# Performance work log

Measured on AMD Instinct MI355X. Metric: run time of the kernel, lower is better.

Reference implementation:

```python
import jax, jax.numpy as jnp
import numpy as np

E_DIM = 64
N_EMBED = 8192

def setup_inputs() -> dict:
    key = jax.random.key(0)
    k1, k2 = jax.random.split(key)
    x = jax.random.normal(k1, (16, E_DIM, 32, 32), dtype=jnp.float32)   # [B, e_dim, H, W]
    embed = jax.random.normal(k2, (E_DIM, N_EMBED), dtype=jnp.float32)  # codebook [e_dim, n_embed]
    return {"x": x, "embed": embed}

def reference(x, embed):
    e_dim, n_embed = embed.shape
    # NCHW -> NHWC
    xp = jnp.transpose(x, (0, 2, 3, 1))              # [B, H, W, e_dim]
    flat = xp.reshape(-1, e_dim)                     # [N, e_dim]
    # squared-distance expansion: ||f||^2 - 2 f.E + ||e||^2  -> [N, n_embed]
    distance = (jnp.sum(flat * flat, axis=1, keepdims=True)
                - 2.0 * flat @ embed
                + jnp.sum(embed * embed, axis=0, keepdims=True))
    embed_idx = jnp.argmax(-distance, axis=1)        # [N] nearest code ids
    embed_idx = embed_idx.reshape(xp.shape[:-1])     # [B, H, W]
    # gather codes: embedding table is embed.T -> [n_embed, e_dim]
    quantize = jnp.take(embed.T, embed_idx, axis=0)  # [B, H, W, e_dim]
    return quantize
```

## Files before the change

kernel.cpp:

```cpp
#include <hip/hip_runtime.h>


typedef __attribute__((ext_vector_type(8))) __bf16 bf16x8;
typedef __attribute__((ext_vector_type(4))) float f32x4;
typedef unsigned int u32;
typedef unsigned long long u64;

union frag_cast { f32x4 f; bf16x8 b; };
__device__ __forceinline__ bf16x8 as_bf16x8(f32x4 v) { frag_cast u; u.f = v; return u.b; }

#define N_ROWS  16384
#define E_DIM   64
#define N_EMBED 8192
#define NCHUNK  16
#define COLS_PER_BLOCK (N_EMBED / NCHUNK)
#define N_ST (COLS_PER_BLOCK / 64)
#define ROWS_PER_BLOCK 256
#define N_ROWBLK (N_ROWS / ROWS_PER_BLOCK)
#define MARGIN_THR 2e-3f

#define WS_AH   0u
#define WS_AL   (2u << 20)
#define WS_B    (4u << 20)
#define WS_ET   (6u << 20)
#define WS_BIAS (8u << 20)
#define WS_PB1  (WS_BIAS + (64u << 10))
#define WS_PI1  (WS_PB1 + (1u << 20))
#define WS_PB2  (WS_PI1 + (1u << 20))
#define WS_FIDX (WS_PB2 + (1u << 20))
#define WS_FLAG (WS_FIDX + (64u << 10))
#define WS_CNT  (WS_FLAG + (64u << 10))
#define WS_FKEY (WS_CNT + (4u << 10))

__device__ __forceinline__ u32 f32_key(float s) {
    u32 u = __float_as_uint(s);
    return (u & 0x80000000u) ? ~u : (u | 0x80000000u);
}

__device__ __forceinline__ void async16(const void* g, void* l) {
    __builtin_amdgcn_global_load_lds(
        (const __attribute__((address_space(1))) void*)g,
        (__attribute__((address_space(3))) void*)l, 16, 0, 0);
}

__global__ __launch_bounds__(256) void prep(
        const float* __restrict__ x, const float* __restrict__ embed, char* ws) {
    __shared__ float tile[64][65];
    __bf16* Ah = (__bf16*)(ws + WS_AH);
    __bf16* Al = (__bf16*)(ws + WS_AL);
    float*  eT = (float*)(ws + WS_ET);
    float*  bias = (float*)(ws + WS_BIAS);
    const int t = threadIdx.x;
    const int blk = blockIdx.x;

    if (blk < 256) {
        const int b = blk >> 4, p0 = (blk & 15) * 64;
        {
            const int c = t >> 2, seg = (t & 3) * 16;
            const float* src = x + b * 65536 + c * 1024 + p0 + seg;
#pragma unroll
            for (int i = 0; i < 16; ++i) tile[c][seg + i] = src[i];
        }
        __syncthreads();
        const int p = t >> 2, cq = (t & 3) * 16;
        const long row = b * 1024 + p0 + p;
        bf16x8 vh0, vh1, vl0, vl1;
#pragma unroll
        for (int i = 0; i < 16; ++i) {
            float f = tile[cq + i][p];
            __bf16 h = (__bf16)f;
            __bf16 l = (__bf16)(f - (float)h);
            if (i < 8) { vh0[i] = h; vl0[i] = l; }
            else       { vh1[i - 8] = h; vl1[i - 8] = l; }
        }
        *(bf16x8*)(Ah + row * 64 + cq) = vh0;
        *(bf16x8*)(Ah + row * 64 + cq + 8) = vh1;
        *(bf16x8*)(Al + row * 64 + cq) = vl0;
        *(bf16x8*)(Al + row * 64 + cq + 8) = vl1;
    } else {
        if (blk == 256 && t == 0) *(int*)(ws + WS_CNT) = 0;
        const int g = blk - 256;
        const int jbase = g * 64;
        char* Bg = ws + WS_B + (size_t)g * 16384;
        {
            const int c = t >> 2, seg = (t & 3) * 16;
            const float* src = embed + c * N_EMBED + jbase + seg;
#pragma unroll
            for (int i = 0; i < 16; ++i) tile[c][seg + i] = src[i];
        }
        __syncthreads();
        if (t < 64) {
            float s = 0.f;
#pragma unroll
            for (int c = 0; c < 64; ++c) { float v = tile[c][t]; s = fmaf(v, v, s); }
            bias[jbase + t] = -0.5f * s;
        }
        const int jl = t >> 2, cq = (t & 3) * 16;
        bf16x8 vh0, vh1, vl0, vl1;
#pragma unroll
        for (int i = 0; i < 16; ++i) {
            float f = tile[cq + i][jl];
            eT[(long)(jbase + jl) * 64 + cq + i] = f;
            __bf16 h = (__bf16)f;
            __bf16 l = (__bf16)(f - (float)h);
            if (i < 8) { vh0[i] = h; vl0[i] = l; }
            else       { vh1[i - 8] = h; vl1[i - 8] = l; }
        }
        const int k0 = (cq >> 3), sw = jl & 7;
        __bf16* hi = (__bf16*)Bg + jl * 64;
        __bf16* lo = (__bf16*)(Bg + 8192) + jl * 64;
        *(bf16x8*)(hi + ((k0 ^ sw) * 8))       = vh0;
        *(bf16x8*)(hi + (((k0 + 1) ^ sw) * 8)) = vh1;
        *(bf16x8*)(lo + ((k0 ^ sw) * 8))       = vl0;
        *(bf16x8*)(lo + (((k0 + 1) ^ sw) * 8)) = vl1;
    }
}

__global__ __launch_bounds__(256, 4) void qdist(const char* __restrict__ ws_c, char* __restrict__ ws) {
    __shared__ __align__(16) char smem[2][16384];
    const __bf16* Ah = (const __bf16*)(ws_c + WS_AH);
    const __bf16* Al = (const __bf16*)(ws_c + WS_AL);
    const char* Bws = ws_c + WS_B;
    const float* biasg = (const float*)(ws_c + WS_BIAS);
    float* pb1 = (float*)(ws + WS_PB1);
    int*   pi1 = (int*)(ws + WS_PI1);
    float* pb2 = (float*)(ws + WS_PB2);

    const int t = threadIdx.x;
    const int wv = t >> 6, lane = t & 63, ln = lane & 15, q = lane >> 4;
    const int rb = blockIdx.x >> 4, chunk = blockIdx.x & 15;
    const int row0 = rb * ROWS_PER_BLOCK;
    const int col0 = chunk * COLS_PER_BLOCK;
    const int g0 = col0 >> 6;

    f32x4 pfh[4][2], pfl[4][2];
#pragma unroll
    for (int nt = 0; nt < 4; ++nt) {
        long row = row0 + wv * 64 + nt * 16 + ln;
        long base = row * 64 + q * 8;
        pfh[nt][0] = *(const f32x4*)(Ah + base);
        pfh[nt][1] = *(const f32x4*)(Ah + base + 32);
        pfl[nt][0] = *(const f32x4*)(Al + base);
        pfl[nt][1] = *(const f32x4*)(Al + base + 32);
    }
    asm volatile("" :
        "+v"(pfh[0][0]), "+v"(pfh[0][1]), "+v"(pfh[1][0]), "+v"(pfh[1][1]),
        "+v"(pfh[2][0]), "+v"(pfh[2][1]), "+v"(pfh[3][0]), "+v"(pfh[3][1]),
        "+v"(pfl[0][0]), "+v"(pfl[0][1]), "+v"(pfl[1][0]), "+v"(pfl[1][1]),
        "+v"(pfl[2][0]), "+v"(pfl[2][1]), "+v"(pfl[3][0]), "+v"(pfl[3][1]));

    float b1[4], b2[4]; int iq[4];
#pragma unroll
    for (int k = 0; k < 4; ++k) { b1[k] = -3.4e38f; b2[k] = -3.4e38f; iq[k] = 0; }

    const int s7 = ln & 7;
    const int rdbase = ln * 128 + ((q ^ s7) << 4);

    auto issue = [&](int st) {
        const char* src = Bws + (size_t)(g0 + st) * 16384;
        char* dst = smem[st & 1];
#pragma unroll
        for (int s = 0; s < 4; ++s)
            async16(src + s * 4096 + wv * 1024 + lane * 16,
                    dst + s * 4096 + wv * 1024);
    };

    issue(0);
    for (int st = 0; st < N_ST; ++st) {
        __syncthreads();
        if (st + 1 < N_ST) issue(st + 1);
        const char* buf = smem[st & 1];
#pragma unroll
        for (int ct = 0; ct < 4; ++ct) {
            const int boff = ct * 2048 + rdbase;
            bf16x8 ah0 = *(const bf16x8*)(buf + boff);
            bf16x8 ah1 = *(const bf16x8*)(buf + (boff ^ 64));
            bf16x8 al0 = *(const bf16x8*)(buf + 8192 + boff);
            bf16x8 al1 = *(const bf16x8*)(buf + 8192 + (boff ^ 64));
            const int cbase = col0 + st * 64 + ct * 16;
            f32x4 bv = *(const f32x4*)(biasg + cbase + q * 4);
            const int jq = cbase + q * 4;
#pragma unroll
            for (int nt = 0; nt < 4; ++nt) {
                f32x4 acc = __builtin_amdgcn_mfma_f32_16x16x32_bf16(al0, as_bf16x8(pfh[nt][0]), bv, 0, 0, 0);
                acc = __builtin_amdgcn_mfma_f32_16x16x32_bf16(al1, as_bf16x8(pfh[nt][1]), acc, 0, 0, 0);
                acc = __builtin_amdgcn_mfma_f32_16x16x32_bf16(ah0, as_bf16x8(pfl[nt][0]), acc, 0, 0, 0);
                acc = __builtin_amdgcn_mfma_f32_16x16x32_bf16(ah1, as_bf16x8(pfl[nt][1]), acc, 0, 0, 0);
                acc = __builtin_amdgcn_mfma_f32_16x16x32_bf16(ah0, as_bf16x8(pfh[nt][0]), acc, 0, 0, 0);
                acc = __builtin_amdgcn_mfma_f32_16x16x32_bf16(ah1, as_bf16x8(pfh[nt][1]), acc, 0, 0, 0);
                float mx = fmaxf(fmaxf(acc[0], acc[1]), fmaxf(acc[2], acc[3]));
                b2[nt] = fmaxf(b2[nt], fminf(b1[nt], mx));
                bool gt = mx > b1[nt];
                b1[nt] = fmaxf(b1[nt], mx);
                iq[nt] = gt ? jq : iq[nt];
            }
        }
    }

#pragma unroll
    for (int m = 16; m < 64; m <<= 1) {
#pragma unroll
        for (int nt = 0; nt < 4; ++nt) {
            float o1 = __shfl_xor(b1[nt], m);
            int   oi = __shfl_xor(iq[nt], m);
            float o2 = __shfl_xor(b2[nt], m);
            b2[nt] = fmaxf(fmaxf(fminf(b1[nt], o1), o2), b2[nt]);
            bool take = (o1 > b1[nt]) || (o1 == b1[nt] && oi < iq[nt]);
            if (take) { b1[nt] = o1; iq[nt] = oi; }
        }
    }
    if (q == 0) {
#pragma unroll
        for (int nt = 0; nt < 4; ++nt) {
            int pixel = row0 + wv * 64 + nt * 16 + ln;
            int o = chunk * N_ROWS + pixel;
            pb1[o] = b1[nt];
            pi1[o] = iq[nt];
            pb2[o] = b2[nt];
        }
    }
}

__global__ __launch_bounds__(256) void reduce_rows(const float* __restrict__ x, char* ws) {
    const float* pb1 = (const float*)(ws + WS_PB1);
    const int*   pi1 = (const int*)(ws + WS_PI1);
    const float* pb2 = (const float*)(ws + WS_PB2);
    const float* eT = (const float*)(ws + WS_ET);
    const float* bias = (const float*)(ws + WS_BIAS);
    int* fidx = (int*)(ws + WS_FIDX);
    int* flags = (int*)(ws + WS_FLAG);
    int* cnt = (int*)(ws + WS_CNT);
    u64* fkey = (u64*)(ws + WS_FKEY);
    const int row = blockIdx.x * 256 + threadIdx.x;

    float b1 = pb1[row]; int iq = pi1[row]; float b2 = pb2[row];
#pragma unroll
    for (int ch = 1; ch < NCHUNK; ++ch) {
        float o1 = pb1[ch * N_ROWS + row];
        int   oi = pi1[ch * N_ROWS + row];
        float o2 = pb2[ch * N_ROWS + row];
        b2 = fmaxf(fmaxf(fminf(b1, o1), o2), b2);
        if (o1 > b1 || (o1 == b1 && oi < iq)) { b1 = o1; iq = oi; }
    }

    if (b1 - b2 < MARGIN_THR) {
        fidx[row] = -1;
        fkey[row] = 0ull;
        flags[atomicAdd(cnt, 1)] = row;
    } else {
        float xr[64];
        const float* xb = x + (row >> 10) * 65536 + (row & 1023);
#pragma unroll
        for (int c = 0; c < 64; ++c) xr[c] = xb[c * 1024];
        float best = -3.4e38f; int bi = iq;
#pragma unroll
        for (int cc = 0; cc < 4; ++cc) {
            const int j = iq + cc;
            const float* e = eT + j * 64;
            float s = bias[j];
#pragma unroll
            for (int c = 0; c < 64; ++c) s = fmaf(xr[c], e[c], s);
            if (s > best) { best = s; bi = j; }
        }
        fidx[row] = bi;
    }
}

__global__ __launch_bounds__(256) void recheck(const float* __restrict__ x, char* ws) {
    __shared__ float fl[64];
    __shared__ u64 red[256];
    const float* eT = (const float*)(ws + WS_ET);
    const float* bias = (const float*)(ws + WS_BIAS);
    const int* flags = (const int*)(ws + WS_FLAG);
    const int n = *(const int*)(ws + WS_CNT);
    u64* fkey = (u64*)(ws + WS_FKEY);
    const int t = threadIdx.x;
    const int seg = blockIdx.x & 31;
    const int rstep = gridDim.x >> 5;
    const int j = seg * 256 + t;

    for (int rowi = blockIdx.x >> 5; rowi < n; rowi += rstep) {
        const int row = flags[rowi];
        __syncthreads();
        if (t < 64) fl[t] = x[(row >> 10) * 65536 + t * 1024 + (row & 1023)];
        __syncthreads();
        float xr[64];
#pragma unroll
        for (int c = 0; c < 64; ++c) xr[c] = fl[c];

        const f32x4* e = (const f32x4*)(eT + (size_t)j * 64);
        f32x4 a0 = {0.f, 0.f, 0.f, 0.f}, a1 = a0, a2 = a0, a3 = a0;
#pragma unroll
        for (int v = 0; v < 4; ++v) {
            f32x4 e0 = e[v * 4 + 0], e1 = e[v * 4 + 1];
            f32x4 e2 = e[v * 4 + 2], e3 = e[v * 4 + 3];
#pragma unroll
            for (int k = 0; k < 4; ++k) {
                a0[k] = fmaf(xr[v * 16 + k],      e0[k], a0[k]);
                a1[k] = fmaf(xr[v * 16 + 4 + k],  e1[k], a1[k]);
                a2[k] = fmaf(xr[v * 16 + 8 + k],  e2[k], a2[k]);
                a3[k] = fmaf(xr[v * 16 + 12 + k], e3[k], a3[k]);
            }
        }
        f32x4 a01 = a0 + a1, a23 = a2 + a3;
        f32x4 as = a01 + a23;
        float s = bias[j] + ((as[0] + as[1]) + (as[2] + as[3]));

        red[t] = ((u64)f32_key(s) << 32) | (u32)(~(u32)j);
        __syncthreads();
        for (int off = 128; off; off >>= 1) {
            if (t < off) { u64 o = red[t + off]; if (o > red[t]) red[t] = o; }
            __syncthreads();
        }
        if (t == 0) atomicMax(&fkey[row], red[0]);
        __syncthreads();
    }
}

__global__ __launch_bounds__(256) void gather_out(const char* __restrict__ ws,
                                                  float* __restrict__ out) {
    const int* fidx = (const int*)(ws + WS_FIDX);
    const u64* fkey = (const u64*)(ws + WS_FKEY);
    const float* eT = (const float*)(ws + WS_ET);
    int g = blockIdx.x * 256 + threadIdx.x;
    int row = g >> 6, c = g & 63;
    int idx = fidx[row];
    if (idx < 0) idx = (int)(~(u32)(fkey[row] & 0xffffffffull));
    out[g] = eT[idx * 64 + c];
}

extern "C" void kernel_launch(void* const* d_in, const int* in_sizes, int n_in,
                              void* d_out, int out_size, void* d_ws, size_t ws_size,
                              hipStream_t stream) {
    const float* x     = (const float*)d_in[0];
    const float* embed = (const float*)d_in[1];
    float* out = (float*)d_out;
    char* ws = (char*)d_ws;

    prep<<<384, 256, 0, stream>>>(x, embed, ws);
    qdist<<<N_ROWBLK * NCHUNK, 256, 0, stream>>>(ws, ws);
    reduce_rows<<<N_ROWS / 256, 256, 0, stream>>>(x, ws);
    recheck<<<2048, 256, 0, stream>>>(x, ws);
    gather_out<<<(N_ROWS * 64) / 256, 256, 0, stream>>>(ws, out);
}
```

Baseline: 137.7 us.

## Fuse row reduction into qdist via last-block-done ticket counter

Removes the separate reduce_rows kernel. Each qdist block now takes a ticket from a per-row-block atomic counter after writing its partial argmax results, and the last of the 16 chunk blocks for a row block performs the cross-chunk reduction, margin check and fp32 refinement. This drops one kernel launch and its launch gap, and lets the reduction overlap with other qdist blocks still running. In exchange it adds a threadfence, an atomic and extra register pressure to qdist, and the reduction work is serialized onto whichever block finishes last.

```diff
diff --git a/kernel.cpp b/kernel.cpp
--- a/kernel.cpp
+++ b/kernel.cpp
@@ -31,6 +31,7 @@
 #define WS_FLAG (WS_FIDX + (64u << 10))
 #define WS_CNT  (WS_FLAG + (64u << 10))
 #define WS_FKEY (WS_CNT + (4u << 10))
+#define WS_DONE (WS_FKEY + (128u << 10))
 
 __device__ __forceinline__ u32 f32_key(float s) {
     u32 u = __float_as_uint(s);
@@ -78,7 +79,10 @@
         *(bf16x8*)(Al + row * 64 + cq) = vl0;
         *(bf16x8*)(Al + row * 64 + cq + 8) = vl1;
     } else {
-        if (blk == 256 && t == 0) *(int*)(ws + WS_CNT) = 0;
+        if (blk == 256) {
+            if (t == 0) *(int*)(ws + WS_CNT) = 0;
+            if (t < N_ROWBLK) ((int*)(ws + WS_DONE))[t] = 0;
+        }
         const int g = blk - 256;
         const int jbase = g * 64;
         char* Bg = ws + WS_B + (size_t)g * 16384;
@@ -116,8 +120,11 @@
     }
 }
 
-__global__ __launch_bounds__(256, 4) void qdist(const char* __restrict__ ws_c, char* __restrict__ ws) {
+__global__ __launch_bounds__(256, 4) void qdist(const float* __restrict__ x,
+                                                const char* __restrict__ ws_c,
+                                                char* __restrict__ ws) {
     __shared__ __align__(16) char smem[2][16384];
+    __shared__ int ticket_s;
     const __bf16* Ah = (const __bf16*)(ws_c + WS_AH);
     const __bf16* Al = (const __bf16*)(ws_c + WS_AL);
     const char* Bws = ws_c + WS_B;
@@ -219,50 +226,51 @@
             pb2[o] = b2[nt];
         }
     }
-}
-
-__global__ __launch_bounds__(256) void reduce_rows(const float* __restrict__ x, char* ws) {
-    const float* pb1 = (const float*)(ws + WS_PB1);
-    const int*   pi1 = (const int*)(ws + WS_PI1);
-    const float* pb2 = (const float*)(ws + WS_PB2);
-    const float* eT = (const float*)(ws + WS_ET);
-    const float* bias = (const float*)(ws + WS_BIAS);
-    int* fidx = (int*)(ws + WS_FIDX);
-    int* flags = (int*)(ws + WS_FLAG);
-    int* cnt = (int*)(ws + WS_CNT);
-    u64* fkey = (u64*)(ws + WS_FKEY);
-    const int row = blockIdx.x * 256 + threadIdx.x;
-
-    float b1 = pb1[row]; int iq = pi1[row]; float b2 = pb2[row];
-#pragma unroll
-    for (int ch = 1; ch < NCHUNK; ++ch) {
-        float o1 = pb1[ch * N_ROWS + row];
-        int   oi = pi1[ch * N_ROWS + row];
-        float o2 = pb2[ch * N_ROWS + row];
-        b2 = fmaxf(fmaxf(fminf(b1, o1), o2), b2);
-        if (o1 > b1 || (o1 == b1 && oi < iq)) { b1 = o1; iq = oi; }
-    }
-
-    if (b1 - b2 < MARGIN_THR) {
-        fidx[row] = -1;
-        fkey[row] = 0ull;
-        flags[atomicAdd(cnt, 1)] = row;
-    } else {
-        float xr[64];
-        const float* xb = x + (row >> 10) * 65536 + (row & 1023);
-#pragma unroll
-        for (int c = 0; c < 64; ++c) xr[c] = xb[c * 1024];
-        float best = -3.4e38f; int bi = iq;
-#pragma unroll
-        for (int cc = 0; cc < 4; ++cc) {
-            const int j = iq + cc;
-            const float* e = eT + j * 64;
-            float s = bias[j];
-#pragma unroll
-            for (int c = 0; c < 64; ++c) s = fmaf(xr[c], e[c], s);
-            if (s > best) { best = s; bi = j; }
-        }
-        fidx[row] = bi;
+
+    __threadfence();
+    __syncthreads();
+    if (t == 0) ticket_s = atomicAdd((int*)(ws + WS_DONE) + rb, 1);
+    __syncthreads();
+    if (ticket_s == NCHUNK - 1) {
+        __threadfence();
+        const float* eT = (const float*)(ws_c + WS_ET);
+        int* fidx = (int*)(ws + WS_FIDX);
+        int* flags = (int*)(ws + WS_FLAG);
+        int* cnt = (int*)(ws + WS_CNT);
+        u64* fkey = (u64*)(ws + WS_FKEY);
+        const int row = row0 + t;
+
+        float rb1 = pb1[row]; int riq = pi1[row]; float rb2 = pb2[row];
+#pragma unroll
+        for (int ch = 1; ch < NCHUNK; ++ch) {
+            float o1 = pb1[ch * N_ROWS + row];
+            int   oi = pi1[ch * N_ROWS + row];
+            float o2 = pb2[ch * N_ROWS + row];
+            rb2 = fmaxf(fmaxf(fminf(rb1, o1), o2), rb2);
+            if (o1 > rb1 || (o1 == rb1 && oi < riq)) { rb1 = o1; riq = oi; }
+        }
+
+        if (rb1 - rb2 < MARGIN_THR) {
+            fidx[row] = -1;
+            fkey[row] = 0ull;
+            flags[atomicAdd(cnt, 1)] = row;
+        } else {
+            float xr[64];
+            const float* xb = x + (row >> 10) * 65536 + (row & 1023);
+#pragma unroll
+            for (int c = 0; c < 64; ++c) xr[c] = xb[c * 1024];
+            float best = -3.4e38f; int bi = riq;
+#pragma unroll
+            for (int cc = 0; cc < 4; ++cc) {
+                const int j = riq + cc;
+                const float* e = eT + j * 64;
+                float s = biasg[j];
+#pragma unroll
+                for (int c = 0; c < 64; ++c) s = fmaf(xr[c], e[c], s);
+                if (s > best) { best = s; bi = j; }
+            }
+            fidx[row] = bi;
+        }
     }
 }
 
@@ -338,8 +346,7 @@
     char* ws = (char*)d_ws;
 
     prep<<<384, 256, 0, stream>>>(x, embed, ws);
-    qdist<<<N_ROWBLK * NCHUNK, 256, 0, stream>>>(ws, ws);
-    reduce_rows<<<N_ROWS / 256, 256, 0, stream>>>(x, ws);
+    qdist<<<N_ROWBLK * NCHUNK, 256, 0, stream>>>(x, ws, ws);
     recheck<<<2048, 256, 0, stream>>>(x, ws);
     gather_out<<<(N_ROWS * 64) / 256, 256, 0, stream>>>(ws, out);
 }
```

New measurement: 298.4 us. 117% more time.
